# Performance work log

Measured on AMD Instinct MI355X. Metric: run time of the kernel, lower is better.

The kernel has to match this reference:

```python
import jax, jax.numpy as jnp
import numpy as np

ADAPTER_RATIO = 0.2


def setup_inputs() -> dict:
    key = jax.random.key(0)
    k1, k2, k3, k4, k5 = jax.random.split(key, 5)
    B, D, R, N_DOM, N_TXT = 16384, 1024, 256, 3, 1380
    image_features = jax.random.normal(k1, (B, D), dtype=jnp.float32)
    domain_labels = jax.random.randint(k2, (B,), 0, N_DOM, dtype=jnp.int64)
    W1 = jax.random.normal(k3, (N_DOM, D, R), dtype=jnp.float32) * 0.02
    W2 = jax.random.normal(k4, (N_DOM, R, D), dtype=jnp.float32) * 0.02
    txt = jax.random.normal(k5, (N_TXT, D), dtype=jnp.float32)
    # text features are L2-normalized at module init (encode_text then norm)
    text_features = txt / jnp.linalg.norm(txt, axis=-1, keepdims=True)
    logit_scale = jnp.asarray(np.log(1.0 / 0.07), dtype=jnp.float32)  # CLIP init
    return {
        "image_features": image_features,
        "domain_labels": domain_labels,
        "W1": W1,
        "W2": W2,
        "text_features": text_features,
        "logit_scale": logit_scale,
    }


def reference(image_features, domain_labels, W1, W2, text_features, logit_scale):
    # Domain-routed adapter MLP: run all n_domains experts (n is tiny), then
    # select the routed output per sample (equivalent to the per-sample loop).
    h = jax.nn.relu(jnp.einsum("bd,ndr->bnr", image_features, W1))  # [B,n,R]
    a = jax.nn.relu(jnp.einsum("bnr,nrd->bnd", h, W2))              # [B,n,D]
    idx = domain_labels[:, None, None]                                # [B,1,1]
    adapter_features = jnp.take_along_axis(a, idx, axis=1)[:, 0, :]   # [B,D]
    fused = ADAPTER_RATIO * adapter_features + (1.0 - ADAPTER_RATIO) * image_features
    fused = fused / jnp.linalg.norm(fused, axis=-1, keepdims=True)
    # text_features already normalized; concat over domains done upstream: [N_TXT, D]
    logits = jnp.exp(logit_scale) * (fused @ text_features.T)         # [B, N_TXT]
    return logits
```

## Files before the change

kernel.cpp:

```cpp
#include <hip/hip_runtime.h>
#include <hip/hip_bf16.h>
#include <math.h>

using bf16 = __hip_bfloat16;
typedef __attribute__((ext_vector_type(8))) short bf16x8;
typedef __attribute__((ext_vector_type(4))) float f32x4;
typedef __attribute__((ext_vector_type(4))) unsigned short us4;

#define GAS __attribute__((address_space(1)))
#define LAS __attribute__((address_space(3)))

__device__ __forceinline__ void gload_lds16(const bf16* g, bf16* lds) {
  __builtin_amdgcn_global_load_lds((const GAS void*)g, (LAS void*)lds, 16, 0, 0);
}
__device__ __forceinline__ float b2f(unsigned short u) {
  union { unsigned short s; bf16 b; } x; x.s = u; return __bfloat162float(x.b);
}
__device__ __forceinline__ unsigned short f2b(float f) {
  union { unsigned short s; bf16 b; } x; x.b = __float2bfloat16(f); return x.s;
}

__global__ __launch_bounds__(256) void hist_k(const int* __restrict__ lab,
                                              int* __restrict__ blockHist) {
  const int blk = blockIdx.x, t = threadIdx.x;
  const int lane = t & 63, w = t >> 6;
  const int d = lab[blk * 256 + t];
  __shared__ int wc[4][3];
#pragma unroll
  for (int dd = 0; dd < 3; ++dd) {
    unsigned long long m = __ballot(d == dd);
    if (lane == 0) wc[w][dd] = __popcll(m);
  }
  __syncthreads();
  if (t < 3) blockHist[blk * 3 + t] = wc[0][t] + wc[1][t] + wc[2][t] + wc[3][t];
}

__global__ __launch_bounds__(256) void scan_k(const int* __restrict__ blockHist,
                                              int* __restrict__ blockOff,
                                              int* __restrict__ meta) {
  __shared__ int h[64][3];
  __shared__ int tot[3];
  const int t = threadIdx.x;
  if (t < 192) h[t / 3][t % 3] = blockHist[t];
  __syncthreads();
  if (t < 3) {
    int s = 0;
    for (int b = 0; b < 64; ++b) { int v = h[b][t]; h[b][t] = s; s += v; }
    tot[t] = s;
    meta[t] = s;
  }
  __syncthreads();
  if (t == 0) { meta[4] = 0; meta[5] = tot[0]; meta[6] = tot[0] + tot[1]; }
  if (t < 192) {
    int b = t / 3, d = t % 3;
    int base = (d == 0) ? 0 : (d == 1 ? tot[0] : tot[0] + tot[1]);
    blockOff[t] = base + h[b][d];
  }
}

__global__ __launch_bounds__(256) void scatter2_k(const int* __restrict__ lab,
                                                  const int* __restrict__ blockOff,
                                                  int* __restrict__ perm) {
  const int blk = blockIdx.x, t = threadIdx.x;
  const int lane = t & 63, w = t >> 6;
  const int i = blk * 256 + t;
  const int d = lab[i];
  __shared__ int wc[4][3];
  unsigned long long mymask = 0;
#pragma unroll
  for (int dd = 0; dd < 3; ++dd) {
    unsigned long long m = __ballot(d == dd);
    if (lane == 0) wc[w][dd] = __popcll(m);
    if (dd == d) mymask = m;
  }
  __syncthreads();
  int woff = 0;
  for (int ww = 0; ww < w; ++ww) woff += wc[ww][d];
  const unsigned long long lt = ((unsigned long long)1 << lane) - 1;
  const int rank = blockOff[blk * 3 + d] + woff + __popcll(mymask & lt);
  perm[rank] = i;
}

__global__ __launch_bounds__(256) void cvt_all_k(const float* __restrict__ x,
                                                 const float* __restrict__ W1,
                                                 const float* __restrict__ W2,
                                                 const float* __restrict__ txt,
                                                 bf16* __restrict__ Xb,
                                                 bf16* __restrict__ W1T,
                                                 bf16* __restrict__ W2T,
                                                 bf16* __restrict__ Tb) {
  int i = blockIdx.x * 256 + threadIdx.x;
  const int nx = 16384 * 1024 / 4;
  if (i < nx) {
    float4 v = ((const float4*)x)[i];
    bf16 t[4] = {__float2bfloat16(v.x), __float2bfloat16(v.y),
                 __float2bfloat16(v.z), __float2bfloat16(v.w)};
    ((us4*)Xb)[i] = *(const us4*)t;
    return;
  }
  int j = i - nx;
  const int n1 = 3 * 256 * 1024;
  const int n2 = n1 + 3 * 1024 * 256;
  const int n3 = n2 + 1536 * 1024;
  if (j < n1) {
    int d = j >> 18, rem = j & 262143;
    int r = rem >> 10, k = rem & 1023;
    W1T[j] = __float2bfloat16(W1[(size_t)d * 262144 + (size_t)k * 256 + r]);
  } else if (j < n2) {
    int jj = j - n1;
    int d = jj >> 18, rem = jj & 262143;
    int n = rem >> 8, k = rem & 255;
    W2T[jj] = __float2bfloat16(W2[(size_t)d * 262144 + (size_t)k * 1024 + n]);
  } else if (j < n3) {
    int jj = j - n2;
    Tb[jj] = (jj < 1380 * 1024) ? __float2bfloat16(txt[jj]) : __float2bfloat16(0.f);
  }
}

template <bool SEG, bool GATHER_A, int EPI>
__global__ __launch_bounds__(256) void gemm_bt(
    const bf16* __restrict__ A, const bf16* __restrict__ BT, bf16* __restrict__ Cv,
    const int* __restrict__ perm, const int* __restrict__ meta, int Mfull, int N,
    int K, int ldc, int Nvalid,
    const float* __restrict__ xf, float* __restrict__ ssp) {
  int cnt = Mfull, base = 0;
  if (SEG) {
    int dom = blockIdx.z;
    cnt = meta[dom];
    base = meta[4 + dom];
    BT += (size_t)dom * N * K;
  }
  const int m0 = blockIdx.x * 128;
  if (m0 >= cnt) return;
  const int n0 = blockIdx.y * 128;

  __shared__ bf16 sA[2][128][32];
  __shared__ bf16 sB[2][128][32];

  const int tid = threadIdx.x;
  const int wid = tid >> 6;
  const int lane = tid & 63;

  const int srow = (wid << 4) + (lane >> 2);
  const int skoff = (((lane & 3) ^ ((lane >> 2) & 3)) << 3);

  int p0 = m0 + srow;       if (p0 > cnt - 1) p0 = cnt - 1;
  int p1 = m0 + srow + 64;  if (p1 > cnt - 1) p1 = cnt - 1;
  long ar0, ar1;
  if (GATHER_A) { ar0 = perm[base + p0]; ar1 = perm[base + p1]; }
  else          { ar0 = base + p0;       ar1 = base + p1; }
  const bf16* a0 = A + (size_t)ar0 * K + skoff;
  const bf16* a1 = A + (size_t)ar1 * K + skoff;
  const bf16* b0 = BT + (size_t)(n0 + srow) * K + skoff;
  const bf16* b1 = BT + (size_t)(n0 + srow + 64) * K + skoff;

  const int fr = lane & 15;
  const int fq = lane >> 4;
  const int rchunk = (fq ^ (fr & 3)) << 3;

  f32x4 acc[4][4];
#pragma unroll
  for (int m = 0; m < 4; ++m)
#pragma unroll
    for (int n = 0; n < 4; ++n) acc[m][n] = (f32x4){0.f, 0.f, 0.f, 0.f};

  const int nk = K >> 5;
  auto stage = [&](int buf, int kt) {
    gload_lds16(a0 + kt * 32, &sA[buf][wid * 16][0]);
    gload_lds16(a1 + kt * 32, &sA[buf][wid * 16 + 64][0]);
    gload_lds16(b0 + kt * 32, &sB[buf][wid * 16][0]);
    gload_lds16(b1 + kt * 32, &sB[buf][wid * 16 + 64][0]);
  };

  stage(0, 0);
  __syncthreads();
  const int wr = wid >> 1, wc = wid & 1;
  for (int kt = 0; kt < nk; ++kt) {
    const int cur = kt & 1;
    if (kt + 1 < nk) stage(cur ^ 1, kt + 1);
    bf16x8 af[4], bfr[4];
#pragma unroll
    for (int m = 0; m < 4; ++m)
      af[m] = *(const bf16x8*)&sA[cur][wr * 64 + m * 16 + fr][rchunk];
#pragma unroll
    for (int n = 0; n < 4; ++n)
      bfr[n] = *(const bf16x8*)&sB[cur][wc * 64 + n * 16 + fr][rchunk];
#pragma unroll
    for (int m = 0; m < 4; ++m)
#pragma unroll
      for (int n = 0; n < 4; ++n)
        acc[m][n] = __builtin_amdgcn_mfma_f32_16x16x32_bf16(af[m], bfr[n], acc[m][n], 0, 0, 0);
    __syncthreads();
  }

  if (EPI == 0) {
#pragma unroll
    for (int m = 0; m < 4; ++m) {
#pragma unroll
      for (int r = 0; r < 4; ++r) {
        const int p = m0 + wr * 64 + m * 16 + fq * 4 + r;
        if (p < cnt) {
          const size_t crow = SEG ? (size_t)(base + p) : (size_t)p;
#pragma unroll
          for (int n = 0; n < 4; ++n) {
            const int col = n0 + wc * 64 + n * 16 + fr;
            if (col < Nvalid)
              Cv[crow * (size_t)ldc + col] = __float2bfloat16(fmaxf(acc[m][n][r], 0.f));
          }
        }
      }
    }
  } else {
    __shared__ float ssred[128][2];
#pragma unroll
    for (int m = 0; m < 4; ++m) {
#pragma unroll
      for (int r = 0; r < 4; ++r) {
        const int lr = wr * 64 + m * 16 + fq * 4 + r;
        const int p = m0 + lr;
        float rowss = 0.f;
        if (p < cnt) {
          const size_t crow = (size_t)perm[base + p];
#pragma unroll
          for (int n = 0; n < 4; ++n) {
            const int col = n0 + wc * 64 + n * 16 + fr;
            const float g = 0.2f * fmaxf(acc[m][n][r], 0.f) + 0.8f * xf[crow * 1024 + col];
            Cv[crow * (size_t)ldc + col] = __float2bfloat16(g);
            rowss += g * g;
          }
        }
        rowss += __shfl_xor(rowss, 1, 16);
        rowss += __shfl_xor(rowss, 2, 16);
        rowss += __shfl_xor(rowss, 4, 16);
        rowss += __shfl_xor(rowss, 8, 16);
        if (fr == 0) ssred[lr][wc] = rowss;
      }
    }
    __syncthreads();
    if (tid < 128) {
      const int p = m0 + tid;
      if (p < cnt) {
        const int crow = perm[base + p];
        ssp[(size_t)blockIdx.y * 16384 + crow] = ssred[tid][0] + ssred[tid][1];
      }
    }
  }
}

__global__ __launch_bounds__(256) void rinv_k(const float* __restrict__ ssp,
                                              float* __restrict__ rinv) {
  const int r = blockIdx.x * 256 + threadIdx.x;
  float s = 0.f;
#pragma unroll
  for (int b = 0; b < 8; ++b) s += ssp[b * 16384 + r];
  rinv[r] = rsqrtf(s);
}

__global__ __launch_bounds__(256, 2) void gemm3_occ(
    const bf16* __restrict__ A, const bf16* __restrict__ BT,
    float* __restrict__ C, const float* __restrict__ scale_ptr,
    const float* __restrict__ rinv) {
  extern __shared__ bf16 smem[];
  bf16* sA0 = smem;
  bf16* sB0 = smem + 16384;

  const int tid = threadIdx.x;
  const int lane = tid & 63, wid = tid >> 6;
  const int wr = wid >> 1, wc = wid & 1;
  const int fr = lane & 15, fq = lane >> 4;

  const int bid = blockIdx.x;
  const int x = bid & 7, seq = bid >> 3;
  const int mb = x * 16 + (seq >> 3), nb = seq & 7;
  const int m0 = mb << 7, n0 = nb * 192;

  auto STAGE = [&](int t) {
    const int s = t & 1, koff = t << 6;
    bf16* da = sA0 + (s << 13);
#pragma unroll
    for (int L = 0; L < 4; ++L) {
      const int idx = (L << 8) + tid;
      const int r = idx >> 3, c = idx & 7;
      gload_lds16(A + (size_t)(m0 + r) * 1024 + koff + ((c ^ (r & 7)) << 3),
                  da + ((idx & ~63) << 3));
    }
    bf16* db = sB0 + s * 12288;
#pragma unroll
    for (int L = 0; L < 6; ++L) {
      const int idx = (L << 8) + tid;
      const int r = idx >> 3, c = idx & 7;
      gload_lds16(BT + (size_t)(n0 + r) * 1024 + koff + ((c ^ (r & 7)) << 3),
                  db + ((idx & ~63) << 3));
    }
  };
  auto LDA = [&](int s, int kk, bf16x8* dst) {
    const bf16* base = sA0 + (s << 13);
#pragma unroll
    for (int m = 0; m < 4; ++m) {
      const int row = (wr << 6) + (m << 4) + fr;
      dst[m] = *(const bf16x8*)(base + (row << 6) + ((((kk << 2) + fq) ^ (fr & 7)) << 3));
    }
  };
  auto LDB = [&](int s, int kk, bf16x8* dst) {
    const bf16* base = sB0 + s * 12288;
#pragma unroll
    for (int n = 0; n < 6; ++n) {
      const int row = wc * 96 + (n << 4) + fr;
      dst[n] = *(const bf16x8*)(base + (row << 6) + ((((kk << 2) + fq) ^ (fr & 7)) << 3));
    }
  };

  f32x4 acc[4][6];
#pragma unroll
  for (int m = 0; m < 4; ++m)
#pragma unroll
    for (int n = 0; n < 6; ++n) acc[m][n] = (f32x4){0.f, 0.f, 0.f, 0.f};

  STAGE(0);
  __syncthreads();
  const int nt = 16;
  for (int t = 0; t < nt; ++t) {
    const int s = t & 1;
    if (t + 1 < nt) STAGE(t + 1);
    bf16x8 a0[4], a1[4], b0[6], b1[6];
    LDA(s, 0, a0); LDB(s, 0, b0);
    LDA(s, 1, a1); LDB(s, 1, b1);
#pragma unroll
    for (int m = 0; m < 4; ++m)
#pragma unroll
      for (int n = 0; n < 6; ++n)
        acc[m][n] = __builtin_amdgcn_mfma_f32_16x16x32_bf16(a0[m], b0[n], acc[m][n], 0, 0, 0);
#pragma unroll
    for (int m = 0; m < 4; ++m)
#pragma unroll
      for (int n = 0; n < 6; ++n)
        acc[m][n] = __builtin_amdgcn_mfma_f32_16x16x32_bf16(a1[m], b1[n], acc[m][n], 0, 0, 0);
    __syncthreads();
  }

  const float sc = expf(*scale_ptr);
#pragma unroll
  for (int m = 0; m < 4; ++m) {
    const int grow = m0 + (wr << 6) + (m << 4) + (fq << 2);
#pragma unroll
    for (int r = 0; r < 4; ++r) {
      const float rv = sc * rinv[grow + r];
#pragma unroll
      for (int n = 0; n < 6; ++n) {
        const int gcol = n0 + wc * 96 + (n << 4) + fr;
        if (gcol < 1380) C[(size_t)(grow + r) * 1380 + gcol] = acc[m][n][r] * rv;
      }
    }
  }
}

extern "C" void kernel_launch(void* const* d_in, const int* in_sizes, int n_in,
                              void* d_out, int out_size, void* d_ws, size_t ws_size,
                              hipStream_t stream) {
  (void)in_sizes; (void)n_in; (void)out_size; (void)ws_size;
  const float* x    = (const float*)d_in[0];
  const int*   lab  = (const int*)d_in[1];
  const float* W1   = (const float*)d_in[2];
  const float* W2   = (const float*)d_in[3];
  const float* text = (const float*)d_in[4];
  const float* lsc  = (const float*)d_in[5];
  float* out = (float*)d_out;

  const int B = 16384, D = 1024, R = 256, NTP = 1536;

  char* p = (char*)d_ws;
  auto carve = [&](size_t bytes) {
    char* r = p;
    p += (bytes + 255) & ~(size_t)255;
    return r;
  };
  int*   meta  = (int*)carve(64);
  int*   bhist = (int*)carve(64 * 3 * 4);
  int*   boff  = (int*)carve(64 * 3 * 4);
  int*   perm  = (int*)carve((size_t)B * 4);
  float* ssp   = (float*)carve((size_t)8 * B * 4);
  float* rinv  = (float*)carve((size_t)B * 4);
  bf16*  Xb    = (bf16*)carve((size_t)B * D * 2);
  bf16*  W1T   = (bf16*)carve((size_t)3 * R * D * 2);
  bf16*  W2T   = (bf16*)carve((size_t)3 * D * R * 2);
  bf16*  Tb    = (bf16*)carve((size_t)NTP * D * 2);
  bf16*  H     = (bf16*)carve((size_t)B * R * 2);
  bf16*  Fb    = (bf16*)carve((size_t)B * D * 2);

  hist_k<<<B / 256, 256, 0, stream>>>(lab, bhist);
  scan_k<<<1, 256, 0, stream>>>(bhist, boff, meta);
  scatter2_k<<<B / 256, 256, 0, stream>>>(lab, boff, perm);

  {
    const int nx = B * D / 4;
    const int total = nx + 3 * R * D + 3 * D * R + NTP * D;
    cvt_all_k<<<(total + 255) / 256, 256, 0, stream>>>(x, W1, W2, text, Xb, W1T, W2T, Tb);
  }

  dim3 g1(128, 2, 3);
  gemm_bt<true, true, 0><<<g1, 256, 0, stream>>>(
      Xb, W1T, H, perm, meta, B, R, D, R, R, nullptr, nullptr);
  dim3 g2(128, 8, 3);
  gemm_bt<true, false, 1><<<g2, 256, 0, stream>>>(
      H, W2T, Fb, perm, meta, B, D, R, D, D, x, ssp);
  rinv_k<<<B / 256, 256, 0, stream>>>(ssp, rinv);
  gemm3_occ<<<1024, 256, 81920, stream>>>(Fb, Tb, out, lsc, rinv);
}
```

Baseline: 169.6 us.

## Fuse rinv into final GEMM, XCD-aware block mapping, grid-stride convert

Removes the separate rinv kernel by having the final GEMM reduce the partial sums of squares into LDS itself. The two adapter GEMMs switch from a 3D grid to a flattened 1D grid, mapped so that blocks sharing an M tile land on the same XCD for L2 reuse. The epilogue now reads bf16 image features instead of fp32, which halves that read traffic but rounds the residual term to bf16. The convert kernel becomes grid-stride with a fixed grid of 4096 blocks.

```diff
diff --git a/kernel.cpp b/kernel.cpp
--- a/kernel.cpp
+++ b/kernel.cpp
@@ -15,9 +15,6 @@
 }
 __device__ __forceinline__ float b2f(unsigned short u) {
   union { unsigned short s; bf16 b; } x; x.s = u; return __bfloat162float(x.b);
-}
-__device__ __forceinline__ unsigned short f2b(float f) {
-  union { unsigned short s; bf16 b; } x; x.b = __float2bfloat16(f); return x.s;
 }
 
 __global__ __launch_bounds__(256) void hist_k(const int* __restrict__ lab,
@@ -89,50 +86,57 @@
                                                  bf16* __restrict__ W1T,
                                                  bf16* __restrict__ W2T,
                                                  bf16* __restrict__ Tb) {
-  int i = blockIdx.x * 256 + threadIdx.x;
   const int nx = 16384 * 1024 / 4;
-  if (i < nx) {
-    float4 v = ((const float4*)x)[i];
-    bf16 t[4] = {__float2bfloat16(v.x), __float2bfloat16(v.y),
-                 __float2bfloat16(v.z), __float2bfloat16(v.w)};
-    ((us4*)Xb)[i] = *(const us4*)t;
-    return;
-  }
-  int j = i - nx;
   const int n1 = 3 * 256 * 1024;
   const int n2 = n1 + 3 * 1024 * 256;
   const int n3 = n2 + 1536 * 1024;
-  if (j < n1) {
-    int d = j >> 18, rem = j & 262143;
-    int r = rem >> 10, k = rem & 1023;
-    W1T[j] = __float2bfloat16(W1[(size_t)d * 262144 + (size_t)k * 256 + r]);
-  } else if (j < n2) {
-    int jj = j - n1;
-    int d = jj >> 18, rem = jj & 262143;
-    int n = rem >> 8, k = rem & 255;
-    W2T[jj] = __float2bfloat16(W2[(size_t)d * 262144 + (size_t)k * 1024 + n]);
-  } else if (j < n3) {
-    int jj = j - n2;
-    Tb[jj] = (jj < 1380 * 1024) ? __float2bfloat16(txt[jj]) : __float2bfloat16(0.f);
-  }
-}
-
-template <bool SEG, bool GATHER_A, int EPI>
+  const int total = nx + n3;
+  for (int i = blockIdx.x * 256 + threadIdx.x; i < total; i += 4096 * 256) {
+    if (i < nx) {
+      float4 v = ((const float4*)x)[i];
+      bf16 t[4] = {__float2bfloat16(v.x), __float2bfloat16(v.y),
+                   __float2bfloat16(v.z), __float2bfloat16(v.w)};
+      ((us4*)Xb)[i] = *(const us4*)t;
+      continue;
+    }
+    int j = i - nx;
+    if (j < n1) {
+      int d = j >> 18, rem = j & 262143;
+      int r = rem >> 10, k = rem & 1023;
+      W1T[j] = __float2bfloat16(W1[(size_t)d * 262144 + (size_t)k * 256 + r]);
+    } else if (j < n2) {
+      int jj = j - n1;
+      int d = jj >> 18, rem = jj & 262143;
+      int n = rem >> 8, k = rem & 255;
+      W2T[jj] = __float2bfloat16(W2[(size_t)d * 262144 + (size_t)k * 1024 + n]);
+    } else {
+      int jj = j - n2;
+      Tb[jj] = (jj < 1380 * 1024) ? __float2bfloat16(txt[jj]) : __float2bfloat16(0.f);
+    }
+  }
+}
+
+template <bool GATHER_A, int EPI, int NBLK>
 __global__ __launch_bounds__(256) void gemm_bt(
     const bf16* __restrict__ A, const bf16* __restrict__ BT, bf16* __restrict__ Cv,
-    const int* __restrict__ perm, const int* __restrict__ meta, int Mfull, int N,
+    const int* __restrict__ perm, const int* __restrict__ meta, int N,
     int K, int ldc, int Nvalid,
-    const float* __restrict__ xf, float* __restrict__ ssp) {
-  int cnt = Mfull, base = 0;
-  if (SEG) {
-    int dom = blockIdx.z;
-    cnt = meta[dom];
-    base = meta[4 + dom];
-    BT += (size_t)dom * N * K;
-  }
-  const int m0 = blockIdx.x * 128;
+    const bf16* __restrict__ xb, float* __restrict__ ssp) {
+  const int bid = blockIdx.x;
+  const int xcd = bid & 7;
+  const int seq = bid >> 3;
+  const int nblkidx = seq % NBLK;
+  const int dm = xcd + 8 * (seq / NBLK);
+  const int dom = dm >> 7;
+  const int mblk = dm & 127;
+
+  const int cnt = meta[dom];
+  const int base = meta[4 + dom];
+  BT += (size_t)dom * N * K;
+
+  const int m0 = mblk * 128;
   if (m0 >= cnt) return;
-  const int n0 = blockIdx.y * 128;
+  const int n0 = nblkidx * 128;
 
   __shared__ bf16 sA[2][128][32];
   __shared__ bf16 sB[2][128][32];
@@ -200,7 +204,7 @@
       for (int r = 0; r < 4; ++r) {
         const int p = m0 + wr * 64 + m * 16 + fq * 4 + r;
         if (p < cnt) {
-          const size_t crow = SEG ? (size_t)(base + p) : (size_t)p;
+          const size_t crow = (size_t)(base + p);
 #pragma unroll
           for (int n = 0; n < 4; ++n) {
             const int col = n0 + wc * 64 + n * 16 + fr;
@@ -224,7 +228,8 @@
 #pragma unroll
           for (int n = 0; n < 4; ++n) {
             const int col = n0 + wc * 64 + n * 16 + fr;
-            const float g = 0.2f * fmaxf(acc[m][n][r], 0.f) + 0.8f * xf[crow * 1024 + col];
+            const float g = 0.2f * fmaxf(acc[m][n][r], 0.f) +
+                            0.8f * b2f(*(const unsigned short*)&xb[crow * 1024 + col]);
             Cv[crow * (size_t)ldc + col] = __float2bfloat16(g);
             rowss += g * g;
           }
@@ -241,25 +246,16 @@
       const int p = m0 + tid;
       if (p < cnt) {
         const int crow = perm[base + p];
-        ssp[(size_t)blockIdx.y * 16384 + crow] = ssred[tid][0] + ssred[tid][1];
+        ssp[(size_t)nblkidx * 16384 + crow] = ssred[tid][0] + ssred[tid][1];
       }
     }
   }
-}
-
-__global__ __launch_bounds__(256) void rinv_k(const float* __restrict__ ssp,
-                                              float* __restrict__ rinv) {
-  const int r = blockIdx.x * 256 + threadIdx.x;
-  float s = 0.f;
-#pragma unroll
-  for (int b = 0; b < 8; ++b) s += ssp[b * 16384 + r];
-  rinv[r] = rsqrtf(s);
 }
 
 __global__ __launch_bounds__(256, 2) void gemm3_occ(
     const bf16* __restrict__ A, const bf16* __restrict__ BT,
     float* __restrict__ C, const float* __restrict__ scale_ptr,
-    const float* __restrict__ rinv) {
+    const float* __restrict__ ssp) {
   extern __shared__ bf16 smem[];
   bf16* sA0 = smem;
   bf16* sB0 = smem + 16384;
@@ -338,13 +334,23 @@
     __syncthreads();
   }
 
+  float* rlds = (float*)smem;
+  if (tid < 128) {
+    float s = 0.f;
+#pragma unroll
+    for (int b = 0; b < 8; ++b) s += ssp[b * 16384 + m0 + tid];
+    rlds[tid] = rsqrtf(s);
+  }
+  __syncthreads();
+
   const float sc = expf(*scale_ptr);
 #pragma unroll
   for (int m = 0; m < 4; ++m) {
-    const int grow = m0 + (wr << 6) + (m << 4) + (fq << 2);
+    const int lrow = (wr << 6) + (m << 4) + (fq << 2);
+    const int grow = m0 + lrow;
 #pragma unroll
     for (int r = 0; r < 4; ++r) {
-      const float rv = sc * rinv[grow + r];
+      const float rv = sc * rlds[lrow + r];
 #pragma unroll
       for (int n = 0; n < 6; ++n) {
         const int gcol = n0 + wc * 96 + (n << 4) + fr;
@@ -379,7 +385,6 @@
   int*   boff  = (int*)carve(64 * 3 * 4);
   int*   perm  = (int*)carve((size_t)B * 4);
   float* ssp   = (float*)carve((size_t)8 * B * 4);
-  float* rinv  = (float*)carve((size_t)B * 4);
   bf16*  Xb    = (bf16*)carve((size_t)B * D * 2);
   bf16*  W1T   = (bf16*)carve((size_t)3 * R * D * 2);
   bf16*  W2T   = (bf16*)carve((size_t)3 * D * R * 2);
@@ -391,18 +396,11 @@
   scan_k<<<1, 256, 0, stream>>>(bhist, boff, meta);
   scatter2_k<<<B / 256, 256, 0, stream>>>(lab, boff, perm);
 
-  {
-    const int nx = B * D / 4;
-    const int total = nx + 3 * R * D + 3 * D * R + NTP * D;
-    cvt_all_k<<<(total + 255) / 256, 256, 0, stream>>>(x, W1, W2, text, Xb, W1T, W2T, Tb);
-  }
-
-  dim3 g1(128, 2, 3);
-  gemm_bt<true, true, 0><<<g1, 256, 0, stream>>>(
-      Xb, W1T, H, perm, meta, B, R, D, R, R, nullptr, nullptr);
-  dim3 g2(128, 8, 3);
-  gemm_bt<true, false, 1><<<g2, 256, 0, stream>>>(
-      H, W2T, Fb, perm, meta, B, D, R, D, D, x, ssp);
-  rinv_k<<<B / 256, 256, 0, stream>>>(ssp, rinv);
-  gemm3_occ<<<1024, 256, 81920, stream>>>(Fb, Tb, out, lsc, rinv);
-}
+  cvt_all_k<<<4096, 256, 0, stream>>>(x, W1, W2, text, Xb, W1T, W2T, Tb);
+
+  gemm_bt<true, 0, 2><<<768, 256, 0, stream>>>(
+      Xb, W1T, H, perm, meta, R, D, R, R, nullptr, nullptr);
+  gemm_bt<false, 1, 8><<<3072, 256, 0, stream>>>(
+      H, W2T, Fb, perm, meta, D, R, D, D, Xb, ssp);
+  gemm3_occ<<<1024, 256, 81920, stream>>>(Fb, Tb, out, lsc, ssp);
+}
```

After: 162.4 us. 4.3% less time.
